# Kernel tuning notes

Measured on AMD Instinct MI355X. Metric: run time of the kernel, lower is better.

Reference implementation:

```python
import jax, jax.numpy as jnp
import numpy as np

PI = 3.14159  # constant used in the torch module
N_QUBITS = 10
N_LAYERS = 4
B = 1024  # number of graphs


def _lin_init(k, fan_in, fan_out):
    k1, k2 = jax.random.split(k)
    s = 1.0 / np.sqrt(fan_in)
    W = jax.random.uniform(k1, (fan_in, fan_out), jnp.float32, -s, s)
    b = jax.random.uniform(k2, (fan_out,), jnp.float32, -s, s)
    return W, b


def setup_inputs():
    key = jax.random.key(0)
    ks = jax.random.split(key, 12)
    N, E, Fin, H, Emb = 32768, 131072, 128, 256, 128
    x = jax.random.normal(ks[0], (N, Fin), jnp.float32)
    edge_index = jax.random.randint(ks[1], (2, E), 0, N)
    batch = jnp.sort(jax.random.randint(ks[2], (N,), 0, B))
    edge_attr = jax.random.uniform(ks[3], (E, 4), dtype=jnp.float32)
    W1, b1 = _lin_init(ks[4], Fin, H)          # GCNConv 1
    W2, b2 = _lin_init(ks[5], H, Emb)          # GCNConv 2
    projW, projb = _lin_init(ks[6], Emb, N_QUBITS)
    vqc_weights = jax.random.uniform(ks[7], (N_LAYERS, N_QUBITS), jnp.float32, 0.0, 2 * np.pi)
    epW, epb = _lin_init(ks[8], 4, N_QUBITS - 1)
    cW1, cb1 = _lin_init(ks[9], Emb + N_QUBITS, 16)
    cW2, cb2 = _lin_init(ks[10], 16, 1)
    return dict(x=x, edge_index=edge_index, batch=batch, edge_attr=edge_attr,
                W1=W1, b1=b1, W2=W2, b2=b2, projW=projW, projb=projb,
                vqc_weights=vqc_weights, epW=epW, epb=epb,
                cW1=cW1, cb1=cb1, cW2=cW2, cb2=cb2)


def _gcn_conv(x, W, b, src, dst, n):
    # GCNConv with self-loops: sym-normalized aggregation of xW
    h = x @ W
    deg = jnp.zeros((n,), x.dtype).at[dst].add(1.0) + 1.0  # +1 self-loop
    dinv = jax.lax.rsqrt(deg)
    coef = (dinv[src] * dinv[dst])[:, None]
    agg = jnp.zeros_like(h).at[dst].add(h[src] * coef)
    return agg + h * (1.0 / deg)[:, None] + b


def _segment_mean(v, seg, n):
    tot = jnp.zeros((n, v.shape[1]), v.dtype).at[seg].add(v)
    cnt = jnp.zeros((n,), v.dtype).at[seg].add(1.0)
    return tot / jnp.clip(cnt, 1.0)[:, None]


def _run_vqc(q_in, weights, ep):
    # Batched real state-vector simulation. All gates (RY, CRY) are real.
    # Wire 0 = most significant bit (pennylane default.qubit convention).
    b = q_in.shape[0]
    dim = 2 ** N_QUBITS
    st = jnp.zeros((b, dim), q_in.dtype).at[:, 0].set(1.0)

    def ry(st, theta, w):
        th = jnp.broadcast_to(theta, (b,)) * 0.5
        c = jnp.cos(th)[:, None, None]
        s = jnp.sin(th)[:, None, None]
        r = st.reshape(b, 2 ** w, 2, -1)
        a0, a1 = r[:, :, 0], r[:, :, 1]
        return jnp.stack([c * a0 - s * a1, s * a0 + c * a1], axis=2).reshape(b, dim)

    def cry(st, theta, w):
        # control w, target w+1 (adjacent wires)
        th = jnp.broadcast_to(theta, (b,)) * 0.5
        c = jnp.cos(th)[:, None, None]
        s = jnp.sin(th)[:, None, None]
        r = st.reshape(b, 2 ** w, 2, 2, -1)
        a0, a1 = r[:, :, 1, 0], r[:, :, 1, 1]
        r = r.at[:, :, 1, 0].set(c * a0 - s * a1).at[:, :, 1, 1].set(s * a0 + c * a1)
        return r.reshape(b, dim)

    for i in range(N_QUBITS):                      # AngleEmbedding (RY)
        st = ry(st, q_in[:, i], i)
    for layer in range(N_LAYERS):
        for i in range(N_QUBITS):
            st = ry(st, weights[layer, i], i)
        for i in range(N_QUBITS - 1):
            st = cry(st, ep[:, i], i)

    probs = st * st
    zs = []
    for i in range(N_QUBITS):
        p = probs.reshape(b, 2 ** i, 2, -1).sum(axis=(1, 3))
        zs.append(p[:, 0] - p[:, 1])               # <PauliZ(i)>
    return jnp.stack(zs, axis=1)                   # [B, n_qubits]


def reference(x, edge_index, batch, edge_attr, W1, b1, W2, b2, projW, projb,
              vqc_weights, epW, epb, cW1, cb1, cW2, cb2):
    N = x.shape[0]
    src, dst = edge_index[0], edge_index[1]
    # GCN encoder: two GCNConv + ReLU, global mean pool (dropout = eval mode)
    h = jax.nn.relu(_gcn_conv(x, W1, b1, src, dst, N))
    h = jax.nn.relu(_gcn_conv(h, W2, b2, src, dst, N))
    emb = _segment_mean(h, batch, B)               # [B, gcn_embed]

    q_in = jnp.tanh(emb @ projW + projb) * PI      # [B, n_qubits]

    # scatter-mean edge pooling per graph, then edge projection
    edge_batch = batch[src]
    pooled_edge = _segment_mean(edge_attr, edge_batch, B)  # [B, 4]
    ep = pooled_edge @ epW + epb                   # [B, n_qubits-1]

    q_out = _run_vqc(q_in, vqc_weights, ep)        # [B, n_qubits]

    combined = jnp.concatenate([emb, q_out], axis=-1)
    hid = jax.nn.relu(combined @ cW1 + cb1)
    return hid @ cW2 + cb2                         # [B, num_tasks]
```

## Files before the change

kernel.cpp:

```cpp
#include <hip/hip_runtime.h>

#define PI_F 3.14159f
#define NQ 10
#define PB 64

__global__ void k_zero(float4* __restrict__ p, int n4) {
  int i = blockIdx.x * blockDim.x + threadIdx.x;
  int stride = gridDim.x * blockDim.x;
  float4 z = {0.f, 0.f, 0.f, 0.f};
  for (; i < n4; i += stride) p[i] = z;
}

__global__ void k_count(const int* __restrict__ dstA, int E, int* __restrict__ cnt) {
  int e = blockIdx.x * blockDim.x + threadIdx.x;
  if (e < E) atomicAdd(&cnt[dstA[e]], 1);
}

__global__ __launch_bounds__(1024) void k_edge_pool(const int* __restrict__ srcA,
                                                    const int* __restrict__ batch,
                                                    const float* __restrict__ eattr, int E,
                                                    float* __restrict__ part) {
  __shared__ float bins[1024 * 5];
  int t = threadIdx.x;
  for (int i = t; i < 5120; i += 1024) bins[i] = 0.f;
  __syncthreads();
  int per = (E + gridDim.x - 1) / gridDim.x;
  int base = blockIdx.x * per;
  int end = min(base + per, E);
  for (int e = base + t; e < end; e += 1024) {
    int s = srcA[e];
    int g = batch[s];
    float4 v = *(const float4*)(eattr + (size_t)e * 4);
    atomicAdd(&bins[g * 5 + 0], v.x);
    atomicAdd(&bins[g * 5 + 1], v.y);
    atomicAdd(&bins[g * 5 + 2], v.z);
    atomicAdd(&bins[g * 5 + 3], v.w);
    atomicAdd(&bins[g * 5 + 4], 1.0f);
  }
  __syncthreads();
  float* dst = part + (size_t)blockIdx.x * 5120;
  for (int i = t; i < 5120; i += 1024) dst[i] = bins[i];
}

__global__ __launch_bounds__(1024) void k_scan1(const int* __restrict__ cnt,
                                                int* __restrict__ incl,
                                                int* __restrict__ bsum) {
  __shared__ int buf[1024];
  int t = threadIdx.x;
  int base = blockIdx.x << 10;
  buf[t] = cnt[base + t];
  __syncthreads();
#pragma unroll
  for (int off = 1; off < 1024; off <<= 1) {
    int x = (t >= off) ? buf[t - off] : 0;
    __syncthreads();
    buf[t] += x;
    __syncthreads();
  }
  incl[base + t] = buf[t];
  if (t == 1023) bsum[blockIdx.x] = buf[t];
}

__global__ void k_node_setup(const int* __restrict__ cnt, const int* __restrict__ incl,
                             const int* __restrict__ bsum, const int* __restrict__ batch,
                             int N, int Bn, int* __restrict__ rowStart,
                             int* __restrict__ pos, float* __restrict__ dinv,
                             float* __restrict__ invdeg, int* __restrict__ starts) {
  int i = blockIdx.x * blockDim.x + threadIdx.x;
  if (i >= N) return;
  int blk = i >> 10;
  int pre = 0;
  for (int j = 0; j < blk; j++) pre += bsum[j];
  int c = cnt[i];
  int inc = incl[i] + pre;
  rowStart[i + 1] = inc;
  pos[i] = inc - c;
  if (i == 0) rowStart[0] = 0;
  float d = (float)c + 1.0f;
  dinv[i] = 1.0f / sqrtf(d);
  invdeg[i] = 1.0f / d;
  int b = batch[i];
  int bp = (i == 0) ? -1 : batch[i - 1];
  for (int g = bp + 1; g <= b; g++) starts[g] = i;
  if (i == N - 1) {
    for (int g = b + 1; g <= Bn; g++) starts[g] = N;
  }
}

__global__ void k_fill(const int* __restrict__ dst, const int* __restrict__ srcA,
                       const float* __restrict__ dinv, int E, int* __restrict__ pos,
                       int* __restrict__ srcSorted, float* __restrict__ dcoef) {
  int e = blockIdx.x * blockDim.x + threadIdx.x;
  if (e >= E) return;
  int s = srcA[e];
  int slot = atomicAdd(&pos[dst[e]], 1);
  srcSorted[slot] = s;
  dcoef[slot] = dinv[s];
}

__global__ __launch_bounds__(256) void k_gemm(const float* __restrict__ A,
                                              const float* __restrict__ B,
                                              float* __restrict__ C,
                                              int M, int K, int N) {
  __shared__ float As[64][36];
  __shared__ float Bs[32][68];
  int t = threadIdx.x;
  int tx = t & 15, ty = t >> 4;
  int row0 = blockIdx.y * 64, col0 = blockIdx.x * 64;
  float acc[4][4] = {};
  for (int k0 = 0; k0 < K; k0 += 32) {
#pragma unroll
    for (int rep = 0; rep < 2; rep++) {
      int slot = t + rep * 256;
      int r = slot >> 3;
      int cg = (slot & 7) << 2;
      float4 v = *(const float4*)(A + (size_t)(row0 + r) * K + (k0 + cg));
      *(float4*)&As[r][cg] = v;
      int r2 = slot >> 4;
      int cg2 = (slot & 15) << 2;
      float4 w = *(const float4*)(B + (size_t)(k0 + r2) * N + (col0 + cg2));
      *(float4*)&Bs[r2][cg2] = w;
    }
    __syncthreads();
#pragma unroll
    for (int kk = 0; kk < 32; kk++) {
      float av[4];
      av[0] = As[ty * 4 + 0][kk];
      av[1] = As[ty * 4 + 1][kk];
      av[2] = As[ty * 4 + 2][kk];
      av[3] = As[ty * 4 + 3][kk];
      float4 b4 = *(const float4*)&Bs[kk][tx << 2];
      float bv[4] = {b4.x, b4.y, b4.z, b4.w};
#pragma unroll
      for (int i = 0; i < 4; i++)
#pragma unroll
        for (int j = 0; j < 4; j++) acc[i][j] = fmaf(av[i], bv[j], acc[i][j]);
    }
    __syncthreads();
  }
#pragma unroll
  for (int i = 0; i < 4; i++) {
    float4 v = {acc[i][0], acc[i][1], acc[i][2], acc[i][3]};
    *(float4*)(C + (size_t)(row0 + ty * 4 + i) * N + (col0 + (tx << 2))) = v;
  }
}

__global__ __launch_bounds__(256) void k_gcn_combine(
    const float* __restrict__ hlin, const int* __restrict__ srcSorted,
    const float* __restrict__ dcoef, const int* __restrict__ rowStart,
    const float* __restrict__ dinv, const float* __restrict__ invdeg,
    const float* __restrict__ bias, float* __restrict__ hout, int N, int C, int shift) {
  int gid = blockIdx.x * blockDim.x + threadIdx.x;
  int n = gid >> shift;
  if (n >= N) return;
  int cq = (gid & ((1 << shift) - 1)) << 2;
  int e0 = rowStart[n], e1 = rowStart[n + 1];
  float di = dinv[n];
  float ax = 0.f, ay = 0.f, az = 0.f, aw = 0.f;
  for (int e = e0; e < e1; e++) {
    int s = srcSorted[e];
    float coef = dcoef[e] * di;
    float4 v = *(const float4*)(hlin + (size_t)s * C + cq);
    ax = fmaf(coef, v.x, ax);
    ay = fmaf(coef, v.y, ay);
    az = fmaf(coef, v.z, az);
    aw = fmaf(coef, v.w, aw);
  }
  float idg = invdeg[n];
  float4 hv = *(const float4*)(hlin + (size_t)n * C + cq);
  float4 bv = *(const float4*)(bias + cq);
  float4 r;
  r.x = fmaxf(fmaf(hv.x, idg, ax) + bv.x, 0.f);
  r.y = fmaxf(fmaf(hv.y, idg, ay) + bv.y, 0.f);
  r.z = fmaxf(fmaf(hv.z, idg, az) + bv.z, 0.f);
  r.w = fmaxf(fmaf(hv.w, idg, aw) + bv.w, 0.f);
  *(float4*)(hout + (size_t)n * C + cq) = r;
}

__device__ __forceinline__ void apply_ry(float* st, int w, float c, float s, int t) {
  int str = 1 << (9 - w);
#pragma unroll
  for (int r = 0; r < 2; r++) {
    int p = t + 256 * r;
    int lo = p & (str - 1);
    int hi = p >> (9 - w);
    int a0 = (hi << (10 - w)) + lo;
    int a1 = a0 + str;
    float x0 = st[a0], x1 = st[a1];
    st[a0] = c * x0 - s * x1;
    st[a1] = s * x0 + c * x1;
  }
}

__device__ __forceinline__ void apply_cry(float* st, int w, float c, float s, int t) {
  int ts = 1 << (8 - w);
  int lo = t & (ts - 1);
  int hi = t >> (8 - w);
  int a0 = (hi << (10 - w)) + (ts << 1) + lo;
  int a1 = a0 + ts;
  float x0 = st[a0], x1 = st[a1];
  st[a0] = c * x0 - s * x1;
  st[a1] = s * x0 + c * x1;
}

__global__ __launch_bounds__(256) void k_vqc_head(
    const float* __restrict__ h2, const int* __restrict__ starts,
    const float* __restrict__ part, const float* __restrict__ projW,
    const float* __restrict__ projb, const float* __restrict__ vqcW,
    const float* __restrict__ epW, const float* __restrict__ epb,
    const float* __restrict__ cW1, const float* __restrict__ cb1,
    const float* __restrict__ cW2, const float* __restrict__ cb2,
    float* __restrict__ out) {
  int g = blockIdx.x;
  int t = threadIdx.x;
  __shared__ float st[1024];
  __shared__ float emb[128];
  __shared__ float csc[59], css[59];
  __shared__ float pool[5];
  __shared__ float zred[4][NQ];
  __shared__ float zq[NQ];
  __shared__ float hid[16];

  int s0 = starts[g], s1 = starts[g + 1];
  int cntn = s1 - s0;
  float invc = 1.0f / (float)(cntn > 0 ? cntn : 1);
  if (t < 128) {
    float sum = 0.f;
    for (int i = s0; i < s1; i++) sum += h2[(size_t)i * 128 + t];
    emb[t] = sum * invc;
  } else if (t >= 192) {
    int lane = t - 192;
    float p0 = 0.f, p1 = 0.f, p2 = 0.f, p3 = 0.f, pc = 0.f;
    for (int b = lane; b < PB; b += 64) {
      const float* pp = part + (size_t)b * 5120 + g * 5;
      p0 += pp[0]; p1 += pp[1]; p2 += pp[2]; p3 += pp[3]; pc += pp[4];
    }
#pragma unroll
    for (int off = 32; off >= 1; off >>= 1) {
      p0 += __shfl_down(p0, off, 64);
      p1 += __shfl_down(p1, off, 64);
      p2 += __shfl_down(p2, off, 64);
      p3 += __shfl_down(p3, off, 64);
      pc += __shfl_down(pc, off, 64);
    }
    if (lane == 0) { pool[0] = p0; pool[1] = p1; pool[2] = p2; pool[3] = p3; pool[4] = pc; }
  }
  st[t] = 0.f; st[t + 256] = 0.f; st[t + 512] = 0.f; st[t + 768] = 0.f;
  __syncthreads();

  if (t < NQ) {
    float sum = projb[t];
    for (int k = 0; k < 128; k++) sum = fmaf(emb[k], projW[k * NQ + t], sum);
    float th = tanhf(sum) * PI_F * 0.5f;
    csc[t] = cosf(th);
    css[t] = sinf(th);
  } else if (t < NQ + 40) {
    float th = vqcW[t - NQ] * 0.5f;
    csc[t] = cosf(th);
    css[t] = sinf(th);
  } else if (t < 59) {
    int i = t - 50;
    float icnt = 1.0f / fmaxf(pool[4], 1.0f);
    float sum = epb[i];
    for (int j = 0; j < 4; j++) sum = fmaf(pool[j] * icnt, epW[j * 9 + i], sum);
    float th = sum * 0.5f;
    csc[t] = cosf(th);
    css[t] = sinf(th);
  }
  if (t == 0) st[0] = 1.0f;
  __syncthreads();

  for (int i = 0; i < NQ; i++) {
    apply_ry(st, i, csc[i], css[i], t);
    __syncthreads();
  }
  for (int L = 0; L < 4; L++) {
    for (int i = 0; i < NQ; i++) {
      apply_ry(st, i, csc[10 + L * 10 + i], css[10 + L * 10 + i], t);
      __syncthreads();
    }
    for (int i = 0; i < NQ - 1; i++) {
      apply_cry(st, i, csc[50 + i], css[50 + i], t);
      __syncthreads();
    }
  }

  float z[NQ];
#pragma unroll
  for (int i = 0; i < NQ; i++) z[i] = 0.f;
#pragma unroll
  for (int r = 0; r < 4; r++) {
    int a = t + 256 * r;
    float p = st[a] * st[a];
#pragma unroll
    for (int i = 0; i < NQ; i++) z[i] += ((a >> (9 - i)) & 1) ? -p : p;
  }
#pragma unroll
  for (int off = 32; off >= 1; off >>= 1) {
#pragma unroll
    for (int i = 0; i < NQ; i++) z[i] += __shfl_down(z[i], off, 64);
  }
  int wave = t >> 6, lane = t & 63;
  if (lane == 0) {
#pragma unroll
    for (int i = 0; i < NQ; i++) zred[wave][i] = z[i];
  }
  __syncthreads();
  if (t < NQ) zq[t] = zred[0][t] + zred[1][t] + zred[2][t] + zred[3][t];
  __syncthreads();

  if (t < 16) {
    float sum = cb1[t];
    for (int k = 0; k < 128; k++) sum = fmaf(emb[k], cW1[k * 16 + t], sum);
    for (int k = 0; k < NQ; k++) sum = fmaf(zq[k], cW1[(128 + k) * 16 + t], sum);
    hid[t] = fmaxf(sum, 0.f);
  }
  __syncthreads();
  if (t == 0) {
    float sum = cb2[0];
    for (int j = 0; j < 16; j++) sum = fmaf(hid[j], cW2[j], sum);
    out[g] = sum;
  }
}

extern "C" void kernel_launch(void* const* d_in, const int* in_sizes, int n_in,
                              void* d_out, int out_size, void* d_ws, size_t ws_size,
                              hipStream_t stream) {
  const float* x = (const float*)d_in[0];
  const int* ei = (const int*)d_in[1];
  const int* batch = (const int*)d_in[2];
  const float* eattr = (const float*)d_in[3];
  const float* W1 = (const float*)d_in[4];
  const float* b1 = (const float*)d_in[5];
  const float* W2 = (const float*)d_in[6];
  const float* b2 = (const float*)d_in[7];
  const float* projW = (const float*)d_in[8];
  const float* projb = (const float*)d_in[9];
  const float* vqcW = (const float*)d_in[10];
  const float* epW = (const float*)d_in[11];
  const float* epb = (const float*)d_in[12];
  const float* cW1 = (const float*)d_in[13];
  const float* cb1 = (const float*)d_in[14];
  const float* cW2 = (const float*)d_in[15];
  const float* cb2 = (const float*)d_in[16];
  float* out = (float*)d_out;

  const int N = in_sizes[0] / 128;
  const int E = in_sizes[1] / 2;
  const int Bn = out_size;

  const int* srcA = ei;
  const int* dstA = ei + E;

  char* ws = (char*)d_ws;
  float* bufA = (float*)ws;
  float* bufB = (float*)(ws + ((size_t)32 << 20));
  size_t off = (size_t)64 << 20;
  auto alloc = [&](size_t bytes) {
    size_t o = off;
    off += (bytes + 255) & ~(size_t)255;
    return o;
  };
  int* cnt = (int*)(ws + alloc((size_t)N * 4));
  size_t zeroEnd = off;
  float* part = (float*)(ws + alloc((size_t)PB * 5120 * 4));
  int* rowStart = (int*)(ws + alloc((size_t)(N + 1) * 4));
  int* pos = (int*)(ws + alloc((size_t)N * 4));
  int* srcSorted = (int*)(ws + alloc((size_t)E * 4));
  float* dcoef = (float*)(ws + alloc((size_t)E * 4));
  float* dinv = (float*)(ws + alloc((size_t)N * 4));
  float* invdeg = (float*)(ws + alloc((size_t)N * 4));
  int* starts = (int*)(ws + alloc((size_t)(Bn + 1) * 4));
  int* incl = (int*)(ws + alloc((size_t)N * 4));
  int* bsum = (int*)(ws + alloc(64 * 4));

  int eblocks = (E + 255) / 256;
  int nblocks = (N + 255) / 256;
  int nb1024 = N >> 10;

  int zero4 = (int)((zeroEnd - ((size_t)64 << 20)) / 16);
  k_zero<<<(zero4 + 255) / 256, 256, 0, stream>>>((float4*)(ws + ((size_t)64 << 20)), zero4);

  k_count<<<eblocks, 256, 0, stream>>>(dstA, E, cnt);
  k_edge_pool<<<PB, 1024, 0, stream>>>(srcA, batch, eattr, E, part);
  k_scan1<<<nb1024, 1024, 0, stream>>>(cnt, incl, bsum);
  k_node_setup<<<nblocks, 256, 0, stream>>>(cnt, incl, bsum, batch, N, Bn, rowStart, pos,
                                            dinv, invdeg, starts);
  k_fill<<<eblocks, 256, 0, stream>>>(dstA, srcA, dinv, E, pos, srcSorted, dcoef);

  {
    dim3 grid(256 / 64, N / 64);
    k_gemm<<<grid, 256, 0, stream>>>(x, W1, bufA, N, 128, 256);
  }
  k_gcn_combine<<<(N * 64) / 256, 256, 0, stream>>>(bufA, srcSorted, dcoef, rowStart,
                                                    dinv, invdeg, b1, bufB, N, 256, 6);
  {
    dim3 grid(128 / 64, N / 64);
    k_gemm<<<grid, 256, 0, stream>>>(bufB, W2, bufA, N, 256, 128);
  }
  k_gcn_combine<<<(N * 32) / 256, 256, 0, stream>>>(bufA, srcSorted, dcoef, rowStart,
                                                    dinv, invdeg, b2, bufB, N, 128, 5);
  k_vqc_head<<<Bn, 256, 0, stream>>>(bufB, starts, part, projW, projb, vqcW, epW,
                                     epb, cW1, cb1, cW2, cb2, out);
}
```

Measured before the change: 193.4 us.

## Simulate VQC state vector in registers with one wave and lane shuffles

The VQC head kernel now keeps the 1024-amplitude state vector in registers, 16 per lane across a single 64-lane wave, instead of in shared memory across 256 threads. Gates on the high wires use __shfl_xor between lanes and gates on the low wires are applied within each lane's registers, so the ~90 __syncthreads barriers between gates go away. Expectation values are reduced with wave shuffles. The cost is four times fewer threads per graph for the embedding mean pooling and a serial dense tail.

New measurement: 202.0 us. 1.04x slower.

```diff
diff --git a/kernel.cpp b/kernel.cpp
--- a/kernel.cpp
+++ b/kernel.cpp
@@ -177,33 +177,93 @@
   *(float4*)(hout + (size_t)n * C + cq) = r;
 }
 
-__device__ __forceinline__ void apply_ry(float* st, int w, float c, float s, int t) {
-  int str = 1 << (9 - w);
-#pragma unroll
-  for (int r = 0; r < 2; r++) {
-    int p = t + 256 * r;
-    int lo = p & (str - 1);
-    int hi = p >> (9 - w);
-    int a0 = (hi << (10 - w)) + lo;
-    int a1 = a0 + str;
-    float x0 = st[a0], x1 = st[a1];
-    st[a0] = c * x0 - s * x1;
-    st[a1] = s * x0 + c * x1;
-  }
-}
-
-__device__ __forceinline__ void apply_cry(float* st, int w, float c, float s, int t) {
-  int ts = 1 << (8 - w);
-  int lo = t & (ts - 1);
-  int hi = t >> (8 - w);
-  int a0 = (hi << (10 - w)) + (ts << 1) + lo;
-  int a1 = a0 + ts;
-  float x0 = st[a0], x1 = st[a1];
-  st[a0] = c * x0 - s * x1;
-  st[a1] = s * x0 + c * x1;
-}
-
-__global__ __launch_bounds__(256) void k_vqc_head(
+
+template <int B>
+__device__ __forceinline__ void ry_reg(float* st, float c, float s) {
+#pragma unroll
+  for (int j = 0; j < 16; j++) {
+    if (!(j & (1 << B))) {
+      float x0 = st[j], x1 = st[j | (1 << B)];
+      st[j] = c * x0 - s * x1;
+      st[j | (1 << B)] = fmaf(s, x0, c * x1);
+    }
+  }
+}
+
+template <int LB>
+__device__ __forceinline__ void ry_lane(float* st, float c, float s, int lane) {
+  bool hi = (lane >> LB) & 1;
+#pragma unroll
+  for (int j = 0; j < 16; j++) {
+    float p = __shfl_xor(st[j], 1 << LB, 64);
+    float a = c * st[j] - s * p;
+    float b = fmaf(s, p, c * st[j]);
+    st[j] = hi ? b : a;
+  }
+}
+
+template <int LC, int LT>
+__device__ __forceinline__ void cry_ll(float* st, float c, float s, int lane) {
+  bool ctrl = (lane >> LC) & 1;
+  bool hi = (lane >> LT) & 1;
+#pragma unroll
+  for (int j = 0; j < 16; j++) {
+    float p = __shfl_xor(st[j], 1 << LT, 64);
+    float a = c * st[j] - s * p;
+    float b = fmaf(s, p, c * st[j]);
+    float nv = hi ? b : a;
+    st[j] = ctrl ? nv : st[j];
+  }
+}
+
+__device__ __forceinline__ void cry_l0r3(float* st, float c, float s, int lane) {
+  bool ctrl = lane & 1;
+#pragma unroll
+  for (int j = 0; j < 8; j++) {
+    float x0 = st[j], x1 = st[j + 8];
+    float n0 = c * x0 - s * x1;
+    float n1 = fmaf(s, x0, c * x1);
+    st[j] = ctrl ? n0 : x0;
+    st[j + 8] = ctrl ? n1 : x1;
+  }
+}
+
+template <int BC, int BT>
+__device__ __forceinline__ void cry_rr(float* st, float c, float s) {
+#pragma unroll
+  for (int j = 0; j < 16; j++) {
+    if ((j & (1 << BC)) && !(j & (1 << BT))) {
+      float x0 = st[j], x1 = st[j | (1 << BT)];
+      st[j] = c * x0 - s * x1;
+      st[j | (1 << BT)] = fmaf(s, x0, c * x1);
+    }
+  }
+}
+
+#define RY_LAYER(base)                                    \
+  ry_lane<5>(st, csc[(base) + 0], css[(base) + 0], lane); \
+  ry_lane<4>(st, csc[(base) + 1], css[(base) + 1], lane); \
+  ry_lane<3>(st, csc[(base) + 2], css[(base) + 2], lane); \
+  ry_lane<2>(st, csc[(base) + 3], css[(base) + 3], lane); \
+  ry_lane<1>(st, csc[(base) + 4], css[(base) + 4], lane); \
+  ry_lane<0>(st, csc[(base) + 5], css[(base) + 5], lane); \
+  ry_reg<3>(st, csc[(base) + 6], css[(base) + 6]);        \
+  ry_reg<2>(st, csc[(base) + 7], css[(base) + 7]);        \
+  ry_reg<1>(st, csc[(base) + 8], css[(base) + 8]);        \
+  ry_reg<0>(st, csc[(base) + 9], css[(base) + 9]);
+
+#define CRY_LAYER()                            \
+  cry_ll<5, 4>(st, csc[50], css[50], lane);    \
+  cry_ll<4, 3>(st, csc[51], css[51], lane);    \
+  cry_ll<3, 2>(st, csc[52], css[52], lane);    \
+  cry_ll<2, 1>(st, csc[53], css[53], lane);    \
+  cry_ll<1, 0>(st, csc[54], css[54], lane);    \
+  cry_l0r3(st, csc[55], css[55], lane);        \
+  cry_rr<3, 2>(st, csc[56], css[56]);          \
+  cry_rr<2, 1>(st, csc[57], css[57]);          \
+  cry_rr<1, 0>(st, csc[58], css[58]);
+
+__global__ __launch_bounds__(64) void k_vqc_head(
     const float* __restrict__ h2, const int* __restrict__ starts,
     const float* __restrict__ part, const float* __restrict__ projW,
     const float* __restrict__ projb, const float* __restrict__ vqcW,
@@ -212,112 +272,115 @@
     const float* __restrict__ cW2, const float* __restrict__ cb2,
     float* __restrict__ out) {
   int g = blockIdx.x;
-  int t = threadIdx.x;
-  __shared__ float st[1024];
-  __shared__ float emb[128];
+  int lane = threadIdx.x;
+  __shared__ float semb[128];
   __shared__ float csc[59], css[59];
   __shared__ float pool[5];
-  __shared__ float zred[4][NQ];
   __shared__ float zq[NQ];
   __shared__ float hid[16];
 
   int s0 = starts[g], s1 = starts[g + 1];
-  int cntn = s1 - s0;
-  float invc = 1.0f / (float)(cntn > 0 ? cntn : 1);
-  if (t < 128) {
-    float sum = 0.f;
-    for (int i = s0; i < s1; i++) sum += h2[(size_t)i * 128 + t];
-    emb[t] = sum * invc;
-  } else if (t >= 192) {
-    int lane = t - 192;
-    float p0 = 0.f, p1 = 0.f, p2 = 0.f, p3 = 0.f, pc = 0.f;
-    for (int b = lane; b < PB; b += 64) {
-      const float* pp = part + (size_t)b * 5120 + g * 5;
-      p0 += pp[0]; p1 += pp[1]; p2 += pp[2]; p3 += pp[3]; pc += pp[4];
-    }
+  float invc = 1.0f / (float)(s1 - s0 > 0 ? s1 - s0 : 1);
+  float e0 = 0.f, e1 = 0.f;
+  for (int i = s0; i < s1; i++) {
+    float2 v = *(const float2*)(h2 + (size_t)i * 128 + lane * 2);
+    e0 += v.x;
+    e1 += v.y;
+  }
+  semb[lane * 2] = e0 * invc;
+  semb[lane * 2 + 1] = e1 * invc;
+
+  {
+    const float* pp = part + (size_t)lane * 5120 + g * 5;
+    float p0 = pp[0], p1 = pp[1], p2 = pp[2], p3 = pp[3], p4 = pp[4];
 #pragma unroll
     for (int off = 32; off >= 1; off >>= 1) {
       p0 += __shfl_down(p0, off, 64);
       p1 += __shfl_down(p1, off, 64);
       p2 += __shfl_down(p2, off, 64);
       p3 += __shfl_down(p3, off, 64);
-      pc += __shfl_down(pc, off, 64);
-    }
-    if (lane == 0) { pool[0] = p0; pool[1] = p1; pool[2] = p2; pool[3] = p3; pool[4] = pc; }
-  }
-  st[t] = 0.f; st[t + 256] = 0.f; st[t + 512] = 0.f; st[t + 768] = 0.f;
-  __syncthreads();
-
-  if (t < NQ) {
-    float sum = projb[t];
-    for (int k = 0; k < 128; k++) sum = fmaf(emb[k], projW[k * NQ + t], sum);
+      p4 += __shfl_down(p4, off, 64);
+    }
+    if (lane == 0) {
+      pool[0] = p0; pool[1] = p1; pool[2] = p2; pool[3] = p3; pool[4] = p4;
+    }
+  }
+  __syncthreads();
+
+  if (lane < NQ) {
+    float sum = projb[lane];
+    for (int k = 0; k < 128; k++) sum = fmaf(semb[k], projW[k * NQ + lane], sum);
     float th = tanhf(sum) * PI_F * 0.5f;
-    csc[t] = cosf(th);
-    css[t] = sinf(th);
-  } else if (t < NQ + 40) {
-    float th = vqcW[t - NQ] * 0.5f;
-    csc[t] = cosf(th);
-    css[t] = sinf(th);
-  } else if (t < 59) {
-    int i = t - 50;
+    csc[lane] = cosf(th);
+    css[lane] = sinf(th);
+  } else if (lane < 50) {
+    float th = vqcW[lane - NQ] * 0.5f;
+    csc[lane] = cosf(th);
+    css[lane] = sinf(th);
+  } else if (lane < 59) {
+    int i = lane - 50;
     float icnt = 1.0f / fmaxf(pool[4], 1.0f);
     float sum = epb[i];
     for (int j = 0; j < 4; j++) sum = fmaf(pool[j] * icnt, epW[j * 9 + i], sum);
     float th = sum * 0.5f;
-    csc[t] = cosf(th);
-    css[t] = sinf(th);
-  }
-  if (t == 0) st[0] = 1.0f;
-  __syncthreads();
-
-  for (int i = 0; i < NQ; i++) {
-    apply_ry(st, i, csc[i], css[i], t);
-    __syncthreads();
-  }
-  for (int L = 0; L < 4; L++) {
-    for (int i = 0; i < NQ; i++) {
-      apply_ry(st, i, csc[10 + L * 10 + i], css[10 + L * 10 + i], t);
-      __syncthreads();
-    }
-    for (int i = 0; i < NQ - 1; i++) {
-      apply_cry(st, i, csc[50 + i], css[50 + i], t);
-      __syncthreads();
-    }
-  }
-
+    csc[lane] = cosf(th);
+    css[lane] = sinf(th);
+  }
+  __syncthreads();
+
+  float st[16];
+#pragma unroll
+  for (int j = 0; j < 16; j++) st[j] = 0.f;
+  if (lane == 0) st[0] = 1.f;
+
+  RY_LAYER(0);
+  RY_LAYER(10); CRY_LAYER();
+  RY_LAYER(20); CRY_LAYER();
+  RY_LAYER(30); CRY_LAYER();
+  RY_LAYER(40); CRY_LAYER();
+
+  float p[16];
+  float tot = 0.f;
+#pragma unroll
+  for (int j = 0; j < 16; j++) {
+    p[j] = st[j] * st[j];
+    tot += p[j];
+  }
   float z[NQ];
 #pragma unroll
-  for (int i = 0; i < NQ; i++) z[i] = 0.f;
-#pragma unroll
-  for (int r = 0; r < 4; r++) {
-    int a = t + 256 * r;
-    float p = st[a] * st[a];
-#pragma unroll
-    for (int i = 0; i < NQ; i++) z[i] += ((a >> (9 - i)) & 1) ? -p : p;
-  }
-#pragma unroll
-  for (int off = 32; off >= 1; off >>= 1) {
-#pragma unroll
-    for (int i = 0; i < NQ; i++) z[i] += __shfl_down(z[i], off, 64);
-  }
-  int wave = t >> 6, lane = t & 63;
+  for (int i = 0; i < 6; i++) {
+    int LB = 5 - i;
+    z[i] = ((lane >> LB) & 1) ? -tot : tot;
+  }
+#pragma unroll
+  for (int i = 6; i < 10; i++) {
+    int B = 9 - i;
+    float a = 0.f;
+#pragma unroll
+    for (int j = 0; j < 16; j++) a += ((j >> B) & 1) ? -p[j] : p[j];
+    z[i] = a;
+  }
+#pragma unroll
+  for (int off = 32; off >= 1; off >>= 1)
+#pragma unroll
+    for (int i = 0; i < 10; i++) z[i] += __shfl_down(z[i], off, 64);
   if (lane == 0) {
 #pragma unroll
-    for (int i = 0; i < NQ; i++) zred[wave][i] = z[i];
-  }
-  __syncthreads();
-  if (t < NQ) zq[t] = zred[0][t] + zred[1][t] + zred[2][t] + zred[3][t];
-  __syncthreads();
-
-  if (t < 16) {
-    float sum = cb1[t];
-    for (int k = 0; k < 128; k++) sum = fmaf(emb[k], cW1[k * 16 + t], sum);
-    for (int k = 0; k < NQ; k++) sum = fmaf(zq[k], cW1[(128 + k) * 16 + t], sum);
-    hid[t] = fmaxf(sum, 0.f);
-  }
-  __syncthreads();
-  if (t == 0) {
+    for (int i = 0; i < 10; i++) zq[i] = z[i];
+  }
+  __syncthreads();
+
+  if (lane < 16) {
+    float sum = cb1[lane];
+    for (int k = 0; k < 128; k++) sum = fmaf(semb[k], cW1[k * 16 + lane], sum);
+#pragma unroll
+    for (int k = 0; k < 10; k++) sum = fmaf(zq[k], cW1[(128 + k) * 16 + lane], sum);
+    hid[lane] = fmaxf(sum, 0.f);
+  }
+  __syncthreads();
+  if (lane == 0) {
     float sum = cb2[0];
+#pragma unroll
     for (int j = 0; j < 16; j++) sum = fmaf(hid[j], cW2[j], sum);
     out[g] = sum;
   }
@@ -400,6 +463,6 @@
   }
   k_gcn_combine<<<(N * 32) / 256, 256, 0, stream>>>(bufA, srcSorted, dcoef, rowStart,
                                                     dinv, invdeg, b2, bufB, N, 128, 5);
-  k_vqc_head<<<Bn, 256, 0, stream>>>(bufB, starts, part, projW, projb, vqcW, epW,
-                                     epb, cW1, cb1, cW2, cb2, out);
-}
+  k_vqc_head<<<Bn, 64, 0, stream>>>(bufB, starts, part, projW, projb, vqcW, epW, epb,
+                                    cW1, cb1, cW2, cb2, out);
+}
```
